# Optimization experiments

Measured on AMD Instinct MI355X. Metric: run time of the kernel, lower is better.

Reference implementation:

```python
import jax, jax.numpy as jnp
import numpy as np

B, N, C = 4, 2048, 1024
H, D = 16, 64  # num_heads, head_dim; C = H*D
R = 16         # lora rank
SCALE = D ** -0.5


def setup_inputs() -> dict:
    key = jax.random.key(0)
    ks = jax.random.split(key, 6)
    return {
        "query": jax.random.normal(ks[0], (B, N, C), dtype=jnp.float32),
        "mask": jax.random.normal(ks[1], (B, 1, N, N), dtype=jnp.float32),
        "W_qkv": jax.random.normal(ks[2], (C, 3 * C), dtype=jnp.float32) * (C ** -0.5),
        "magnitude": jnp.ones((1, H, 1, 1), dtype=jnp.float32),
        "W_loraA": jax.random.normal(ks[3], (C, R), dtype=jnp.float32) * (C ** -0.5),
        "W_loraB": jax.random.normal(ks[4], (R, C), dtype=jnp.float32) * (R ** -0.5),
        "W_proj": jax.random.normal(ks[5], (C, C), dtype=jnp.float32) * (C ** -0.5),
    }


def reference(query, mask, W_qkv, magnitude, W_loraA, W_loraB, W_proj):
    # qkv projection: [B,N,3C] -> [3,B,H,N,D]
    qkv = (query @ W_qkv).reshape(B, N, 3, H, D).transpose(2, 0, 3, 1, 4)
    q, k, v = qkv[0], qkv[1], qkv[2]
    # LoRA/DoRA delta fused into q before attention
    delta = (query @ W_loraA) @ W_loraB                     # [B,N,C]
    delta = delta.reshape(B, N, H, D).transpose(0, 2, 1, 3)  # [B,H,N,D]
    q = q + magnitude * delta
    # attention
    attn = jnp.einsum('bhnd,bhmd->bhnm', q, k) * SCALE + mask
    attn = jax.nn.softmax(attn, axis=-1)
    out = jnp.einsum('bhnm,bhmd->bhnd', attn, v)            # [B,H,N,D]
    out = out.transpose(0, 2, 1, 3).reshape(B, N, C)
    return out @ W_proj
```

## Files before the change

kernel.cpp:

```cpp
#include <hip/hip_runtime.h>
#include <hip/hip_bf16.h>

#define Bd 4
#define Nd 2048
#define Cd 1024
#define Hd 16
#define Dd 64
#define Rd 16
#define KAUG 1056
#define SCALEf 0.125f
#define PIT 72

using short8 = __attribute__((ext_vector_type(8))) short;
using f32x4  = __attribute__((ext_vector_type(4))) float;

static __device__ __forceinline__ ushort f2bf(float f) {
    __hip_bfloat16 h = __float2bfloat16(f);
    return *reinterpret_cast<ushort*>(&h);
}

#define GLOAD_LDS16(g, l) __builtin_amdgcn_global_load_lds( \
    (const __attribute__((address_space(1))) void*)(g),      \
    (__attribute__((address_space(3))) void*)(l), 16, 0, 0)

__global__ __launch_bounds__(256) void pack_a_kernel(
    const float* __restrict__ query, ushort* __restrict__ Aaug)
{
    const int row = blockIdx.x;
    const int t = threadIdx.x;
    const float4 v = *(const float4*)&query[(size_t)row * Cd + t * 4];
    ushort4 u;
    u.x = f2bf(v.x); u.y = f2bf(v.y); u.z = f2bf(v.z); u.w = f2bf(v.w);
    *(ushort4*)&Aaug[(size_t)row * KAUG + t * 4] = u;
}

__global__ __launch_bounds__(256) void pack_wat_kernel(
    const float* __restrict__ WA, ushort* __restrict__ WAT)
{
    const int idx = blockIdx.x * 256 + threadIdx.x;
    const int c = idx >> 4, r = idx & 15;
    WAT[r * 1024 + c] = f2bf(WA[idx]);
}

__global__ __launch_bounds__(64) void lora_mfma_kernel(
    const ushort* __restrict__ Aro, const ushort* __restrict__ WAT,
    ushort* __restrict__ Awr)
{
    const int lane = threadIdx.x;
    const int quad = lane >> 4, lc = lane & 15;
    const int row0 = blockIdx.x * 16;
    f32x4 acc = {0.f, 0.f, 0.f, 0.f};
    #pragma unroll 4
    for (int k0 = 0; k0 < 1024; k0 += 32) {
        const short8 a = *(const short8*)&Aro[(size_t)(row0 + lc) * KAUG + k0 + quad * 8];
        const short8 b = *(const short8*)&WAT[lc * 1024 + k0 + quad * 8];
        acc = __builtin_amdgcn_mfma_f32_16x16x32_bf16(a, b, acc, 0, 0, 0);
    }
    #pragma unroll
    for (int ri = 0; ri < 4; ++ri) {
        const size_t row = row0 + quad * 4 + ri;
        Awr[row * KAUG + 1024 + lc] = f2bf(acc[ri]);
        Awr[row * KAUG + 1040 + lc] = 0;
    }
}

__global__ __launch_bounds__(256) void pack_bqkv_kernel(
    const float* __restrict__ Wqkv, const float* __restrict__ WloraB,
    const float* __restrict__ magnitude, ushort* __restrict__ BT)
{
    __shared__ float tile[32][33];
    const int k0 = blockIdx.x * 32, n0 = blockIdx.y * 32;
    const int tx = threadIdx.x & 31, ty = threadIdx.x >> 5;
    #pragma unroll
    for (int i = 0; i < 4; ++i) {
        const int k = k0 + ty + i * 8;
        const int n = n0 + tx;
        float v;
        if (k < 1024)                      v = Wqkv[(size_t)k * 3072 + n];
        else if (k < 1040 && n < 1024)     v = magnitude[n >> 6] * WloraB[(k - 1024) * Cd + n];
        else                               v = 0.f;
        tile[ty + i * 8][tx] = v;
    }
    __syncthreads();
    #pragma unroll
    for (int i = 0; i < 4; ++i) {
        const int n = n0 + ty + i * 8;
        const int k = k0 + tx;
        BT[(size_t)n * KAUG + k] = f2bf(tile[tx][ty + i * 8]);
    }
}

__global__ __launch_bounds__(256) void pack_bproj_kernel(
    const float* __restrict__ Wp, ushort* __restrict__ BT)
{
    __shared__ float tile[32][33];
    const int k0 = blockIdx.x * 32, n0 = blockIdx.y * 32;
    const int tx = threadIdx.x & 31, ty = threadIdx.x >> 5;
    #pragma unroll
    for (int i = 0; i < 4; ++i)
        tile[ty + i * 8][tx] = Wp[(size_t)(k0 + ty + i * 8) * Cd + n0 + tx];
    __syncthreads();
    #pragma unroll
    for (int i = 0; i < 4; ++i)
        BT[(size_t)(n0 + ty + i * 8) * Cd + k0 + tx] = f2bf(tile[tx][ty + i * 8]);
}

template <int KD, int MODE>
__global__ __launch_bounds__(256) void mfma_gemm_kernel(
    const ushort* __restrict__ Ag, const ushort* __restrict__ Bg,
    ushort* __restrict__ qb, ushort* __restrict__ kb, ushort* __restrict__ vb,
    float* __restrict__ outf)
{
    __shared__ ushort As[128 * 32];
    __shared__ ushort Bs[128 * 32];
    const int t = threadIdx.x;
    const int w = t >> 6, lane = t & 63, quad = lane >> 4, lc = lane & 15;
    const int wm = w >> 1, wn = w & 1;
    const int m0 = blockIdx.y * 128, n0 = blockIdx.x * 128;

    f32x4 acc[4][4] = {};

    const int lin0 = t, lin1 = t + 256;
    const int rowT0 = lin0 >> 2, kc0 = (lin0 & 3) * 8;
    const int rowT1 = lin1 >> 2, kc1 = (lin1 & 3) * 8;

    for (int k0 = 0; k0 < KD; k0 += 32) {
        GLOAD_LDS16(&Ag[(size_t)(m0 + rowT0) * KD + k0 + kc0], &As[lin0 * 8]);
        GLOAD_LDS16(&Ag[(size_t)(m0 + rowT1) * KD + k0 + kc1], &As[lin1 * 8]);
        GLOAD_LDS16(&Bg[(size_t)(n0 + rowT0) * KD + k0 + kc0], &Bs[lin0 * 8]);
        GLOAD_LDS16(&Bg[(size_t)(n0 + rowT1) * KD + k0 + kc1], &Bs[lin1 * 8]);
        __syncthreads();
        short8 a[4], b[4];
        #pragma unroll
        for (int i = 0; i < 4; ++i)
            a[i] = *(const short8*)&As[(wm * 64 + i * 16 + lc) * 32 + quad * 8];
        #pragma unroll
        for (int j = 0; j < 4; ++j)
            b[j] = *(const short8*)&Bs[(wn * 64 + j * 16 + lc) * 32 + quad * 8];
        #pragma unroll
        for (int i = 0; i < 4; ++i)
            #pragma unroll
            for (int j = 0; j < 4; ++j)
                acc[i][j] = __builtin_amdgcn_mfma_f32_16x16x32_bf16(a[i], b[j], acc[i][j], 0, 0, 0);
        __syncthreads();
    }

    if (MODE == 0) {
        const int sec = n0 >> 10;
        ushort* dst = sec == 0 ? qb : (sec == 1 ? kb : vb);
        #pragma unroll
        for (int i = 0; i < 4; ++i)
            #pragma unroll
            for (int j = 0; j < 4; ++j) {
                const int gcol = (n0 & 1023) + wn * 64 + j * 16 + lc;
                const int h = gcol >> 6, d = gcol & 63;
                #pragma unroll
                for (int r = 0; r < 4; ++r) {
                    const int grow = m0 + wm * 64 + i * 16 + quad * 4 + r;
                    const int b_ = grow >> 11, n_ = grow & 2047;
                    dst[(((size_t)(b_ * Hd) + h) * Nd + n_) * Dd + d] = f2bf(acc[i][j][r]);
                }
            }
    } else {
        #pragma unroll
        for (int i = 0; i < 4; ++i)
            #pragma unroll
            for (int j = 0; j < 4; ++j) {
                const int gcol = n0 + wn * 64 + j * 16 + lc;
                #pragma unroll
                for (int r = 0; r < 4; ++r) {
                    const int grow = m0 + wm * 64 + i * 16 + quad * 4 + r;
                    outf[(size_t)grow * Cd + gcol] = acc[i][j][r];
                }
            }
    }
}

__global__ __launch_bounds__(256) void attn_mfma_kernel(
    const ushort* __restrict__ qbuf, const ushort* __restrict__ kbuf,
    const ushort* __restrict__ vbuf, const float* __restrict__ mask,
    ushort* __restrict__ attn_out)
{
    __shared__ short Ks[2][64 * PIT];
    __shared__ short Vts[2][64 * PIT];
    __shared__ short Ps[128 * PIT];

    const int t = threadIdx.x;
    const int w = t >> 6, lane = t & 63;
    const int quad = lane >> 4, lc = lane & 15;
    const int bh = blockIdx.y, b = bh >> 4, h = bh & 15;
    const int n0 = blockIdx.x * 128;

    const short* qg = (const short*)qbuf + (size_t)bh * Nd * Dd;
    const short* kg = (const short*)kbuf + (size_t)bh * Nd * Dd;
    const short* vg = (const short*)vbuf + (size_t)bh * Nd * Dd;
    const float* mbase = mask + ((size_t)b * Nd + n0) * Nd;

    short8 qf[2][2];
    #pragma unroll
    for (int sub = 0; sub < 2; ++sub)
        #pragma unroll
        for (int ks = 0; ks < 2; ++ks)
            qf[sub][ks] = *(const short8*)
                &qg[(size_t)(n0 + w * 32 + sub * 16 + lc) * Dd + ks * 32 + quad * 8];

    float rs[2][4];
    f32x4 o[2][4];
    #pragma unroll
    for (int sub = 0; sub < 2; ++sub)
        #pragma unroll
        for (int dt = 0; dt < 4; ++dt) {
            o[sub][dt] = (f32x4){0.f, 0.f, 0.f, 0.f};
            rs[sub][dt] = 0.f;
        }

    const int krow = t >> 2, kcol = (t & 3) * 16;
    const int kv0 = (t >> 3) * 2, dgv = t & 7, d0v = dgv * 8;
    const int vblk = ((kv0 >> 3) ^ dgv) & 7;

    int4 kr0, kr1, vr0, vr1;
    kr0 = *(const int4*)&kg[(size_t)krow * Dd + kcol];
    kr1 = *(const int4*)&kg[(size_t)krow * Dd + kcol + 8];
    vr0 = *(const int4*)&vg[(size_t)kv0 * Dd + d0v];
    vr1 = *(const int4*)&vg[(size_t)(kv0 + 1) * Dd + d0v];
    *(int4*)&Ks[0][krow * PIT + kcol]     = kr0;
    *(int4*)&Ks[0][krow * PIT + kcol + 8] = kr1;
    {
        ushort u0[8], u1[8];
        *(int4*)u0 = vr0; *(int4*)u1 = vr1;
        #pragma unroll
        for (int i = 0; i < 8; ++i)
            *(uint*)&Vts[0][(d0v + i) * PIT + vblk * 8 + (kv0 & 7)] =
                (uint)u0[i] | ((uint)u1[i] << 16);
    }
    kr0 = *(const int4*)&kg[(size_t)(64 + krow) * Dd + kcol];
    kr1 = *(const int4*)&kg[(size_t)(64 + krow) * Dd + kcol + 8];
    vr0 = *(const int4*)&vg[(size_t)(64 + kv0) * Dd + d0v];
    vr1 = *(const int4*)&vg[(size_t)(64 + kv0 + 1) * Dd + d0v];
    __syncthreads();

    for (int m0 = 0; m0 < Nd; m0 += 64) {
        const int c = (m0 >> 6) & 1;
        float mk0[4][4];
        #pragma unroll
        for (int r = 0; r < 4; ++r)
            #pragma unroll
            for (int nt = 0; nt < 4; ++nt)
                mk0[r][nt] = mbase[(size_t)(w * 32 + quad * 4 + r) * Nd
                                   + m0 + nt * 16 + lc];

        f32x4 s[2][4];
        #pragma unroll
        for (int sub = 0; sub < 2; ++sub)
            #pragma unroll
            for (int nt = 0; nt < 4; ++nt)
                s[sub][nt] = (f32x4){0.f, 0.f, 0.f, 0.f};
        __builtin_amdgcn_s_setprio(1);
        #pragma unroll
        for (int ks = 0; ks < 2; ++ks)
            #pragma unroll
            for (int nt = 0; nt < 4; ++nt) {
                const short8 kf = *(const short8*)
                    &Ks[c][(nt * 16 + lc) * PIT + ks * 32 + quad * 8];
                s[0][nt] = __builtin_amdgcn_mfma_f32_16x16x32_bf16(qf[0][ks], kf, s[0][nt], 0, 0, 0);
                s[1][nt] = __builtin_amdgcn_mfma_f32_16x16x32_bf16(qf[1][ks], kf, s[1][nt], 0, 0, 0);
            }
        __builtin_amdgcn_s_setprio(0);

        *(int4*)&Ks[c ^ 1][krow * PIT + kcol]     = kr0;
        *(int4*)&Ks[c ^ 1][krow * PIT + kcol + 8] = kr1;
        const int mnx = (m0 + 128) & (Nd - 1);
        kr0 = *(const int4*)&kg[(size_t)(mnx + krow) * Dd + kcol];
        kr1 = *(const int4*)&kg[(size_t)(mnx + krow) * Dd + kcol + 8];

        float mk1[4][4];
        #pragma unroll
        for (int r = 0; r < 4; ++r)
            #pragma unroll
            for (int nt = 0; nt < 4; ++nt)
                mk1[r][nt] = mbase[(size_t)(w * 32 + 16 + quad * 4 + r) * Nd
                                   + m0 + nt * 16 + lc];

        {
            const int rowg = w * 32 + quad * 4;
            #pragma unroll
            for (int nt = 0; nt < 4; ++nt) {
                const int cbx = ((nt * 2 + (lc >> 3)) ^ quad) * 8 + (lc & 7);
                const float p0 = __expf(fmaf(s[0][nt][0], SCALEf, mk0[0][nt]));
                const float p1 = __expf(fmaf(s[0][nt][1], SCALEf, mk0[1][nt]));
                const float p2 = __expf(fmaf(s[0][nt][2], SCALEf, mk0[2][nt]));
                const float p3 = __expf(fmaf(s[0][nt][3], SCALEf, mk0[3][nt]));
                rs[0][0] += p0; rs[0][1] += p1; rs[0][2] += p2; rs[0][3] += p3;
                uint pk01, pk23;
                asm("v_cvt_pk_bf16_f32 %0, %1, %2" : "=v"(pk01) : "v"(p0), "v"(p1));
                asm("v_cvt_pk_bf16_f32 %0, %1, %2" : "=v"(pk23) : "v"(p2), "v"(p3));
                Ps[(rowg + 0) * PIT + cbx] = (short)pk01;
                Ps[(rowg + 1) * PIT + cbx] = (short)(pk01 >> 16);
                Ps[(rowg + 2) * PIT + cbx] = (short)pk23;
                Ps[(rowg + 3) * PIT + cbx] = (short)(pk23 >> 16);
            }
        }
        {
            const int rowg = w * 32 + 16 + quad * 4;
            #pragma unroll
            for (int nt = 0; nt < 4; ++nt) {
                const int cbx = ((nt * 2 + (lc >> 3)) ^ quad) * 8 + (lc & 7);
                const float p0 = __expf(fmaf(s[1][nt][0], SCALEf, mk1[0][nt]));
                const float p1 = __expf(fmaf(s[1][nt][1], SCALEf, mk1[1][nt]));
                const float p2 = __expf(fmaf(s[1][nt][2], SCALEf, mk1[2][nt]));
                const float p3 = __expf(fmaf(s[1][nt][3], SCALEf, mk1[3][nt]));
                rs[1][0] += p0; rs[1][1] += p1; rs[1][2] += p2; rs[1][3] += p3;
                uint pk01, pk23;
                asm("v_cvt_pk_bf16_f32 %0, %1, %2" : "=v"(pk01) : "v"(p0), "v"(p1));
                asm("v_cvt_pk_bf16_f32 %0, %1, %2" : "=v"(pk23) : "v"(p2), "v"(p3));
                Ps[(rowg + 0) * PIT + cbx] = (short)pk01;
                Ps[(rowg + 1) * PIT + cbx] = (short)(pk01 >> 16);
                Ps[(rowg + 2) * PIT + cbx] = (short)pk23;
                Ps[(rowg + 3) * PIT + cbx] = (short)(pk23 >> 16);
            }
        }
        __builtin_amdgcn_s_setprio(1);
        #pragma unroll
        for (int ks = 0; ks < 2; ++ks) {
            short8 bb[4];
            #pragma unroll
            for (int dt = 0; dt < 4; ++dt) {
                const int d = dt * 16 + lc;
                const int blk = (ks * 4 + quad) ^ ((d >> 3) & 7);
                bb[dt] = *(const short8*)&Vts[c][d * PIT + blk * 8];
            }
            const int pblk = (((ks * 4 + quad) ^ ((lc >> 2) & 3)) & 7) * 8;
            #pragma unroll
            for (int sub = 0; sub < 2; ++sub) {
                const short8 a = *(const short8*)&Ps[(w * 32 + sub * 16 + lc) * PIT + pblk];
                #pragma unroll
                for (int dt = 0; dt < 4; ++dt)
                    o[sub][dt] = __builtin_amdgcn_mfma_f32_16x16x32_bf16(a, bb[dt], o[sub][dt], 0, 0, 0);
            }
        }
        __builtin_amdgcn_s_setprio(0);

        {
            ushort u0[8], u1[8];
            *(int4*)u0 = vr0; *(int4*)u1 = vr1;
            #pragma unroll
            for (int i = 0; i < 8; ++i)
                *(uint*)&Vts[c ^ 1][(d0v + i) * PIT + vblk * 8 + (kv0 & 7)] =
                    (uint)u0[i] | ((uint)u1[i] << 16);
        }
        vr0 = *(const int4*)&vg[(size_t)(mnx + kv0) * Dd + d0v];
        vr1 = *(const int4*)&vg[(size_t)(mnx + kv0 + 1) * Dd + d0v];

        __syncthreads();
    }

    #pragma unroll
    for (int sub = 0; sub < 2; ++sub) {
        const int rowg = w * 32 + sub * 16 + quad * 4;
        #pragma unroll
        for (int r = 0; r < 4; ++r) {
            float v = rs[sub][r];
            v += __shfl_xor(v, 1);
            v += __shfl_xor(v, 2);
            v += __shfl_xor(v, 4);
            v += __shfl_xor(v, 8);
            const float inv = 1.f / v;
            const size_t rowo = ((size_t)(b * Nd + n0 + rowg + r)) * Cd + h * Dd;
            #pragma unroll
            for (int dt = 0; dt < 4; ++dt)
                attn_out[rowo + dt * 16 + lc] = f2bf(o[sub][dt][r] * inv);
        }
    }
}

extern "C" void kernel_launch(void* const* d_in, const int* in_sizes, int n_in,
                              void* d_out, int out_size, void* d_ws, size_t ws_size,
                              hipStream_t stream) {
    const float* query     = (const float*)d_in[0];
    const float* mask      = (const float*)d_in[1];
    const float* Wqkv      = (const float*)d_in[2];
    const float* magnitude = (const float*)d_in[3];
    const float* WloraA    = (const float*)d_in[4];
    const float* WloraB    = (const float*)d_in[5];
    const float* Wproj     = (const float*)d_in[6];
    float* out = (float*)d_out;

    const size_t SZ = (size_t)Bd * Hd * Nd * Dd;
    char* p = (char*)d_ws;
    ushort* qbuf = (ushort*)p;           p += SZ * 2;
    ushort* kbuf = (ushort*)p;           p += SZ * 2;
    ushort* vbuf = (ushort*)p;           p += SZ * 2;
    ushort* aout = (ushort*)p;           p += SZ * 2;
    ushort* Aaug = (ushort*)p;           p += (size_t)8192 * KAUG * 2;
    ushort* BT   = (ushort*)p;           p += (size_t)3072 * KAUG * 2;
    ushort* WpT  = (ushort*)p;           p += (size_t)1024 * 1024 * 2;
    ushort* WAT  = (ushort*)p;           p += (size_t)16 * 1024 * 2;

    pack_a_kernel<<<dim3(Bd * Nd), 256, 0, stream>>>(query, Aaug);
    pack_wat_kernel<<<dim3(64), 256, 0, stream>>>(WloraA, WAT);
    pack_bqkv_kernel<<<dim3(KAUG / 32, 3072 / 32), 256, 0, stream>>>(
        Wqkv, WloraB, magnitude, BT);
    pack_bproj_kernel<<<dim3(32, 32), 256, 0, stream>>>(Wproj, WpT);
    lora_mfma_kernel<<<dim3(512), 64, 0, stream>>>(Aaug, WAT, Aaug);
    mfma_gemm_kernel<KAUG, 0><<<dim3(24, 64), 256, 0, stream>>>(
        Aaug, BT, qbuf, kbuf, vbuf, nullptr);
    attn_mfma_kernel<<<dim3(Nd / 128, Bd * Hd), 256, 0, stream>>>(
        qbuf, kbuf, vbuf, mask, aout);
    mfma_gemm_kernel<1024, 1><<<dim3(8, 64), 256, 0, stream>>>(
        aout, WpT, nullptr, nullptr, nullptr, out);
}
```

Before: 384.7 us.

## Fuse pack kernels into one launch and use K=64 swizzled LDS GEMM tiles

After: 372.5 us. 3.2% less time.

```diff
diff --git a/kernel.cpp b/kernel.cpp
--- a/kernel.cpp
+++ b/kernel.cpp
@@ -7,7 +7,7 @@
 #define Hd 16
 #define Dd 64
 #define Rd 16
-#define KAUG 1056
+#define KAUG 1088
 #define SCALEf 0.125f
 #define PIT 72
 
@@ -23,23 +23,60 @@
     (const __attribute__((address_space(1))) void*)(g),      \
     (__attribute__((address_space(3))) void*)(l), 16, 0, 0)
 
-__global__ __launch_bounds__(256) void pack_a_kernel(
-    const float* __restrict__ query, ushort* __restrict__ Aaug)
+__global__ __launch_bounds__(256) void pack_fused_kernel(
+    const float* __restrict__ query, ushort* __restrict__ Aaug,
+    const float* __restrict__ WA, ushort* __restrict__ WAT,
+    const float* __restrict__ Wqkv, const float* __restrict__ WloraB,
+    const float* __restrict__ magnitude, ushort* __restrict__ BT,
+    const float* __restrict__ Wp, ushort* __restrict__ WpT)
 {
-    const int row = blockIdx.x;
+    __shared__ float tile[32][33];
+    const int bid = blockIdx.x;
     const int t = threadIdx.x;
-    const float4 v = *(const float4*)&query[(size_t)row * Cd + t * 4];
-    ushort4 u;
-    u.x = f2bf(v.x); u.y = f2bf(v.y); u.z = f2bf(v.z); u.w = f2bf(v.w);
-    *(ushort4*)&Aaug[(size_t)row * KAUG + t * 4] = u;
-}
-
-__global__ __launch_bounds__(256) void pack_wat_kernel(
-    const float* __restrict__ WA, ushort* __restrict__ WAT)
-{
-    const int idx = blockIdx.x * 256 + threadIdx.x;
-    const int c = idx >> 4, r = idx & 15;
-    WAT[r * 1024 + c] = f2bf(WA[idx]);
+
+    if (bid < 8192) {
+        const int row = bid;
+        const float4 v = *(const float4*)&query[(size_t)row * Cd + t * 4];
+        ushort4 u;
+        u.x = f2bf(v.x); u.y = f2bf(v.y); u.z = f2bf(v.z); u.w = f2bf(v.w);
+        *(ushort4*)&Aaug[(size_t)row * KAUG + t * 4] = u;
+    } else if (bid < 8256) {
+        const int idx = (bid - 8192) * 256 + t;
+        const int c = idx >> 4, r = idx & 15;
+        WAT[r * 1024 + c] = f2bf(WA[idx]);
+    } else if (bid < 11520) {
+        const int sub = bid - 8256;
+        const int k0 = (sub % 34) * 32, n0 = (sub / 34) * 32;
+        const int tx = t & 31, ty = t >> 5;
+        #pragma unroll
+        for (int i = 0; i < 4; ++i) {
+            const int k = k0 + ty + i * 8;
+            const int n = n0 + tx;
+            float v;
+            if (k < 1024)                      v = Wqkv[(size_t)k * 3072 + n];
+            else if (k < 1040 && n < 1024)     v = magnitude[n >> 6] * WloraB[(k - 1024) * Cd + n];
+            else                               v = 0.f;
+            tile[ty + i * 8][tx] = v;
+        }
+        __syncthreads();
+        #pragma unroll
+        for (int i = 0; i < 4; ++i) {
+            const int n = n0 + ty + i * 8;
+            const int k = k0 + tx;
+            BT[(size_t)n * KAUG + k] = f2bf(tile[tx][ty + i * 8]);
+        }
+    } else {
+        const int sub = bid - 11520;
+        const int k0 = (sub % 32) * 32, n0 = (sub / 32) * 32;
+        const int tx = t & 31, ty = t >> 5;
+        #pragma unroll
+        for (int i = 0; i < 4; ++i)
+            tile[ty + i * 8][tx] = Wp[(size_t)(k0 + ty + i * 8) * Cd + n0 + tx];
+        __syncthreads();
+        #pragma unroll
+        for (int i = 0; i < 4; ++i)
+            WpT[(size_t)(n0 + ty + i * 8) * Cd + k0 + tx] = f2bf(tile[tx][ty + i * 8]);
+    }
 }
 
 __global__ __launch_bounds__(64) void lora_mfma_kernel(
@@ -61,48 +98,9 @@
         const size_t row = row0 + quad * 4 + ri;
         Awr[row * KAUG + 1024 + lc] = f2bf(acc[ri]);
         Awr[row * KAUG + 1040 + lc] = 0;
-    }
-}
-
-__global__ __launch_bounds__(256) void pack_bqkv_kernel(
-    const float* __restrict__ Wqkv, const float* __restrict__ WloraB,
-    const float* __restrict__ magnitude, ushort* __restrict__ BT)
-{
-    __shared__ float tile[32][33];
-    const int k0 = blockIdx.x * 32, n0 = blockIdx.y * 32;
-    const int tx = threadIdx.x & 31, ty = threadIdx.x >> 5;
-    #pragma unroll
-    for (int i = 0; i < 4; ++i) {
-        const int k = k0 + ty + i * 8;
-        const int n = n0 + tx;
-        float v;
-        if (k < 1024)                      v = Wqkv[(size_t)k * 3072 + n];
-        else if (k < 1040 && n < 1024)     v = magnitude[n >> 6] * WloraB[(k - 1024) * Cd + n];
-        else                               v = 0.f;
-        tile[ty + i * 8][tx] = v;
-    }
-    __syncthreads();
-    #pragma unroll
-    for (int i = 0; i < 4; ++i) {
-        const int n = n0 + ty + i * 8;
-        const int k = k0 + tx;
-        BT[(size_t)n * KAUG + k] = f2bf(tile[tx][ty + i * 8]);
-    }
-}
-
-__global__ __launch_bounds__(256) void pack_bproj_kernel(
-    const float* __restrict__ Wp, ushort* __restrict__ BT)
-{
-    __shared__ float tile[32][33];
-    const int k0 = blockIdx.x * 32, n0 = blockIdx.y * 32;
-    const int tx = threadIdx.x & 31, ty = threadIdx.x >> 5;
-    #pragma unroll
-    for (int i = 0; i < 4; ++i)
-        tile[ty + i * 8][tx] = Wp[(size_t)(k0 + ty + i * 8) * Cd + n0 + tx];
-    __syncthreads();
-    #pragma unroll
-    for (int i = 0; i < 4; ++i)
-        BT[(size_t)(n0 + ty + i * 8) * Cd + k0 + tx] = f2bf(tile[tx][ty + i * 8]);
+        Awr[row * KAUG + 1056 + lc] = 0;
+        Awr[row * KAUG + 1072 + lc] = 0;
+    }
 }
 
 template <int KD, int MODE>
@@ -111,8 +109,8 @@
     ushort* __restrict__ qb, ushort* __restrict__ kb, ushort* __restrict__ vb,
     float* __restrict__ outf)
 {
-    __shared__ ushort As[128 * 32];
-    __shared__ ushort Bs[128 * 32];
+    __shared__ ushort As[128 * 64];
+    __shared__ ushort Bs[128 * 64];
     const int t = threadIdx.x;
     const int w = t >> 6, lane = t & 63, quad = lane >> 4, lc = lane & 15;
     const int wm = w >> 1, wn = w & 1;
@@ -120,28 +118,38 @@
 
     f32x4 acc[4][4] = {};
 
-    const int lin0 = t, lin1 = t + 256;
-    const int rowT0 = lin0 >> 2, kc0 = (lin0 & 3) * 8;
-    const int rowT1 = lin1 >> 2, kc1 = (lin1 & 3) * 8;
-
-    for (int k0 = 0; k0 < KD; k0 += 32) {
-        GLOAD_LDS16(&Ag[(size_t)(m0 + rowT0) * KD + k0 + kc0], &As[lin0 * 8]);
-        GLOAD_LDS16(&Ag[(size_t)(m0 + rowT1) * KD + k0 + kc1], &As[lin1 * 8]);
-        GLOAD_LDS16(&Bg[(size_t)(n0 + rowT0) * KD + k0 + kc0], &Bs[lin0 * 8]);
-        GLOAD_LDS16(&Bg[(size_t)(n0 + rowT1) * KD + k0 + kc1], &Bs[lin1 * 8]);
+    for (int k0 = 0; k0 < KD; k0 += 64) {
+        #pragma unroll
+        for (int p = 0; p < 4; ++p) {
+            const int idx = t + p * 256;
+            const int row = idx >> 3;
+            const int cb  = idx & 7;
+            const int gc  = cb ^ (row & 7);
+            GLOAD_LDS16(&Ag[(size_t)(m0 + row) * KD + k0 + gc * 8], &As[idx * 8]);
+            GLOAD_LDS16(&Bg[(size_t)(n0 + row) * KD + k0 + gc * 8], &Bs[idx * 8]);
+        }
         __syncthreads();
-        short8 a[4], b[4];
-        #pragma unroll
-        for (int i = 0; i < 4; ++i)
-            a[i] = *(const short8*)&As[(wm * 64 + i * 16 + lc) * 32 + quad * 8];
-        #pragma unroll
-        for (int j = 0; j < 4; ++j)
-            b[j] = *(const short8*)&Bs[(wn * 64 + j * 16 + lc) * 32 + quad * 8];
-        #pragma unroll
-        for (int i = 0; i < 4; ++i)
-            #pragma unroll
-            for (int j = 0; j < 4; ++j)
-                acc[i][j] = __builtin_amdgcn_mfma_f32_16x16x32_bf16(a[i], b[j], acc[i][j], 0, 0, 0);
+        #pragma unroll
+        for (int ks = 0; ks < 2; ++ks) {
+            short8 a[4], b[4];
+            #pragma unroll
+            for (int i = 0; i < 4; ++i) {
+                const int r = wm * 64 + i * 16 + lc;
+                const int xc = (ks * 4 + quad) ^ (lc & 7);
+                a[i] = *(const short8*)&As[r * 64 + xc * 8];
+            }
+            #pragma unroll
+            for (int j = 0; j < 4; ++j) {
+                const int r = wn * 64 + j * 16 + lc;
+                const int xc = (ks * 4 + quad) ^ (lc & 7);
+                b[j] = *(const short8*)&Bs[r * 64 + xc * 8];
+            }
+            #pragma unroll
+            for (int i = 0; i < 4; ++i)
+                #pragma unroll
+                for (int j = 0; j < 4; ++j)
+                    acc[i][j] = __builtin_amdgcn_mfma_f32_16x16x32_bf16(a[i], b[j], acc[i][j], 0, 0, 0);
+        }
         __syncthreads();
     }
 
@@ -396,11 +404,8 @@
     ushort* WpT  = (ushort*)p;           p += (size_t)1024 * 1024 * 2;
     ushort* WAT  = (ushort*)p;           p += (size_t)16 * 1024 * 2;
 
-    pack_a_kernel<<<dim3(Bd * Nd), 256, 0, stream>>>(query, Aaug);
-    pack_wat_kernel<<<dim3(64), 256, 0, stream>>>(WloraA, WAT);
-    pack_bqkv_kernel<<<dim3(KAUG / 32, 3072 / 32), 256, 0, stream>>>(
-        Wqkv, WloraB, magnitude, BT);
-    pack_bproj_kernel<<<dim3(32, 32), 256, 0, stream>>>(Wproj, WpT);
+    pack_fused_kernel<<<dim3(12544), 256, 0, stream>>>(
+        query, Aaug, WloraA, WAT, Wqkv, WloraB, magnitude, BT, Wproj, WpT);
     lora_mfma_kernel<<<dim3(512), 64, 0, stream>>>(Aaug, WAT, Aaug);
     mfma_gemm_kernel<KAUG, 0><<<dim3(24, 64), 256, 0, stream>>>(
         Aaug, BT, qbuf, kbuf, vbuf, nullptr);
```
